# Performance work log

Measured on AMD Instinct MI355X. Metric: run time of the kernel, lower is better.

## Reference

```python
import jax, jax.numpy as jnp
import numpy as np

B, N, FEAT, D = 8, 2048, 64, 6
RADIUS, NSAMPLE, TOPK, NHEAD, NLAYER = 0.3, 64, 16, 8, 2
EPS = 1e-5


def _bn(x, p, axis=1):
    # eval-mode batchnorm; p rows = (gamma, beta, running_mean, running_var)
    g, b, m, v = p
    sh = [1] * x.ndim
    sh[axis] = -1
    rs = lambda t: t.reshape(sh)
    return (x - rs(m)) * (rs(g) / jnp.sqrt(rs(v) + EPS)) + rs(b)


def _ln(x, g, b):
    mu = jnp.mean(x, -1, keepdims=True)
    var = jnp.mean((x - mu) ** 2, -1, keepdims=True)
    return (x - mu) / jnp.sqrt(var + EPS) * g + b


def _mha(x, w_in, b_in, w_out, b_out):
    bsz, n, e = x.shape
    hd = e // NHEAD
    qkv = x @ w_in.T + b_in                      # [B,N,3E]
    q, k, v = jnp.split(qkv, 3, axis=-1)
    sp = lambda t: t.reshape(bsz, n, NHEAD, hd).transpose(0, 2, 1, 3)  # [B,H,N,hd]
    q, k, v = sp(q), sp(k), sp(v)
    att = jax.nn.softmax(jnp.einsum('bhnd,bhmd->bhnm', q, k) * (1.0 / hd ** 0.5), axis=-1)
    o = jnp.einsum('bhnm,bhmd->bhnd', att, v).transpose(0, 2, 1, 3).reshape(bsz, n, e)
    return o @ w_out.T + b_out


def _forward(sortvec, input, tl_win, tl_bin, tl_wout, tl_bout, tl_w1, tl_b1, tl_w2, tl_b2,
             tl_ln1g, tl_ln1b, tl_ln2g, tl_ln2b,
             fg_w0, fg_b0, fg_w1, fg_b1, fg_w2, fg_b2, fbn0, fbn1, fbn2,
             rc_w0, rc_b0, rc_w1, rc_b1, rc_w2, rc_b2, rbn0, rbn1, rbn2,
             fl_w0, fl_b0, fl_w1, fl_b1, lbn0, lbn1):
    b = sortvec.shape[0]
    n = sortvec.shape[-1]
    relu = jax.nn.relu

    # --- input self-attention (2 post-norm TransformerEncoder layers) ---
    x = sortvec[:, 0].transpose(0, 2, 1)         # [B,N,FEAT]
    for l in range(NLAYER):
        a = _mha(x, tl_win[l], tl_bin[l], tl_wout[l], tl_bout[l])
        x = _ln(x + a, tl_ln1g[l], tl_ln1b[l])
        f = relu(x @ tl_w1[l].T + tl_b1[l]) @ tl_w2[l].T + tl_b2[l]
        x = _ln(x + f, tl_ln2g[l], tl_ln2b[l])

    # --- feat_generator (RFFNet: Conv2d(FEAT,1) then 1x1 convs) + BN + relu ---
    s = jnp.einsum('cf,bnf->bcn', fg_w0, x) + fg_b0[:, None]   # [B,64,N]
    s = relu(_bn(s, fbn0))
    s = relu(_bn(jnp.einsum('co,bon->bcn', fg_w1, s) + fg_b1[:, None], fbn1))
    s = relu(_bn(jnp.einsum('co,bon->bcn', fg_w2, s) + fg_b2[:, None], fbn2))
    scores = s[:, 0]                              # [B,N]

    # --- top-k point selection ---
    _, idx = jax.lax.top_k(scores, TOPK)          # [B,K]
    all_points = input.transpose(0, 2, 1)         # [B,N,6]
    bidx = jnp.arange(b)[:, None]
    query = all_points[bidx, idx]                 # [B,K,6]

    # --- query_ball_point (PointNet++ style) ---
    xyz, qxyz = all_points[..., :3], query[..., :3]
    sqr = jnp.sum((qxyz[:, :, None, :] - xyz[:, None, :, :]) ** 2, -1)   # [B,K,N]
    gidx = jnp.where(sqr > RADIUS ** 2, n, jnp.arange(n)[None, None, :])
    gidx = jnp.sort(gidx, axis=-1)[..., :NSAMPLE]                        # [B,K,S]
    gidx = jnp.where(gidx == n, gidx[..., :1], gidx)
    radius_points = all_points[jnp.arange(b)[:, None, None], gidx]       # [B,K,S,6]
    grouped = jnp.concatenate([query[:, :, None, :], radius_points], axis=2)  # [B,K,S+1,6]

    # --- radius_cnn (Conv3d (1,S+1,6) then 1x1x1) + BN3d + relu ---
    r = jnp.einsum('cpd,bkpd->bck', rc_w0, grouped) + rc_b0[:, None]     # [B,128,K]
    r = relu(_bn(r, rbn0))
    r = relu(_bn(jnp.einsum('co,bok->bck', rc_w1, r) + rc_b1[:, None], rbn1))
    r = relu(_bn(jnp.einsum('co,bok->bck', rc_w2, r) + rc_b2[:, None], rbn2))  # [B,512,K]

    # --- flatten + Linear/BN1d/relu chain ---
    h = r.reshape(b, -1)                          # [B, 512*K]
    h = relu(_bn(h @ fl_w0.T + fl_b0, lbn0))
    h = relu(_bn(h @ fl_w1.T + fl_b1, lbn1))
    return h[..., None], idx                      # [B,512,1], [B,K]


def setup_inputs() -> dict:
    key = jax.random.key(0)
    ks = iter(jax.random.split(key, 80))
    rnd = lambda shape, s=0.02: jax.random.normal(next(ks), shape, jnp.float32) * s

    def bn_p(c):
        g = 1.0 + rnd((c,))
        bb = rnd((c,))
        m = rnd((c,))
        v = 1.0 + 0.1 * jnp.abs(rnd((c,), 1.0))
        return jnp.stack([g, bb, m, v])

    F = FEAT
    return dict(
        sortvec=jax.random.normal(next(ks), (B, 1, F, N), jnp.float32),
        input=jax.random.normal(next(ks), (B, D, N), jnp.float32),
        tl_win=rnd((NLAYER, 3 * F, F)), tl_bin=rnd((NLAYER, 3 * F)),
        tl_wout=rnd((NLAYER, F, F)), tl_bout=rnd((NLAYER, F)),
        tl_w1=rnd((NLAYER, 2048, F)), tl_b1=rnd((NLAYER, 2048)),
        tl_w2=rnd((NLAYER, F, 2048)), tl_b2=rnd((NLAYER, F)),
        tl_ln1g=jnp.ones((NLAYER, F)), tl_ln1b=jnp.zeros((NLAYER, F)),
        tl_ln2g=jnp.ones((NLAYER, F)), tl_ln2b=jnp.zeros((NLAYER, F)),
        fg_w0=rnd((64, F), 0.1), fg_b0=jnp.zeros((64,)),
        fg_w1=rnd((16, 64), 0.1), fg_b1=jnp.zeros((16,)),
        fg_w2=rnd((1, 16), 0.1), fg_b2=jnp.zeros((1,)),
        fbn0=bn_p(64), fbn1=bn_p(16), fbn2=bn_p(1),
        rc_w0=rnd((128, NSAMPLE + 1, D), 0.05), rc_b0=jnp.zeros((128,)),
        rc_w1=rnd((256, 128), 0.05), rc_b1=jnp.zeros((256,)),
        rc_w2=rnd((512, 256), 0.05), rc_b2=jnp.zeros((512,)),
        rbn0=bn_p(128), rbn1=bn_p(256), rbn2=bn_p(512),
        fl_w0=rnd((1024, 512 * TOPK), 0.02), fl_b0=jnp.zeros((1024,)),
        fl_w1=rnd((512, 1024), 0.02), fl_b1=jnp.zeros((512,)),
        lbn0=bn_p(1024), lbn1=bn_p(512),
    )


def reference(sortvec, input, tl_win, tl_bin, tl_wout, tl_bout, tl_w1, tl_b1, tl_w2, tl_b2,
              tl_ln1g, tl_ln1b, tl_ln2g, tl_ln2b,
              fg_w0, fg_b0, fg_w1, fg_b1, fg_w2, fg_b2, fbn0, fbn1, fbn2,
              rc_w0, rc_b0, rc_w1, rc_b1, rc_w2, rc_b2, rbn0, rbn1, rbn2,
              fl_w0, fl_b0, fl_w1, fl_b1, lbn0, lbn1):
    return _forward(sortvec, input, tl_win, tl_bin, tl_wout, tl_bout, tl_w1, tl_b1, tl_w2, tl_b2,
                    tl_ln1g, tl_ln1b, tl_ln2g, tl_ln2b,
                    fg_w0, fg_b0, fg_w1, fg_b1, fg_w2, fg_b2, fbn0, fbn1, fbn2,
                    rc_w0, rc_b0, rc_w1, rc_b1, rc_w2, rc_b2, rbn0, rbn1, rbn2,
                    fl_w0, fl_b0, fl_w1, fl_b1, lbn0, lbn1)
```

## Files before the change

### kernel.cpp

```cpp
#include <hip/hip_runtime.h>
#include <hip/hip_bf16.h>
#include <math.h>

#define BB 8
#define NN 2048
#define FF 64
#define DD 6
#define NSAMP 64
#define TOPK 16
#define NHEAD 8
#define HD 8
#define NLAYER 2
#define EPSF 1e-5f
#define R2 0.09f

typedef short short8 __attribute__((ext_vector_type(8)));
typedef float f32x4 __attribute__((ext_vector_type(4)));
typedef unsigned int u32;

__device__ inline unsigned pk2(float x) {
  unsigned b = __float_as_uint(x);
  unsigned hi = (b + 0x7fffu + ((b >> 16) & 1u)) >> 16;
  float r = x - __uint_as_float(hi << 16);
  unsigned c = __float_as_uint(r);
  unsigned lo = (c + 0x7fffu + ((c >> 16) & 1u)) >> 16;
  return (hi << 16) | lo;
}

__device__ inline unsigned short bf16r(float x) {
  unsigned b = __float_as_uint(x);
  return (unsigned short)((b + 0x7fffu + ((b >> 16) & 1u)) >> 16);
}

__device__ __forceinline__ void gl16(const void* g, void* l) {
  __builtin_amdgcn_global_load_lds((const __attribute__((address_space(1))) u32*)g,
                                   (__attribute__((address_space(3))) u32*)l, 16, 0, 0);
}

__global__ void k_transpose(const float* __restrict__ sv, float* __restrict__ x) {
  int i = blockIdx.x * 256 + threadIdx.x;
  if (i >= BB * NN * FF) return;
  int f = i % FF;
  int n = (i / FF) % NN;
  int b = i / (FF * NN);
  x[i] = sv[(b * FF + f) * NN + n];
}

__global__ void k_wimg(const float* __restrict__ w1, const float* __restrict__ w2,
                       unsigned short* __restrict__ img) {
  int i = blockIdx.x * 256 + threadIdx.x;
  int e = i & 4095;
  int plane = (i >> 12) & 3;
  int chg = (i >> 14) & 31;
  int l = i >> 19;
  int r = e >> 6, sh = (e >> 3) & 7, inner = e & 7;
  int s = sh ^ (r & 7);
  float v;
  if (plane < 2) v = w1[((size_t)(l * 2048 + chg * 64 + r)) * 64 + s * 8 + inner];
  else           v = w2[((size_t)(l * 64 + r)) * 2048 + chg * 64 + s * 8 + inner];
  unsigned p = pk2(v);
  img[i] = (unsigned short)((plane & 1) ? (p & 0xffffu) : (p >> 16));
}

__global__ void k_qkv3(const float* __restrict__ x, const float* __restrict__ win,
                       const float* __restrict__ bin, float* __restrict__ qbuf,
                       uint4* __restrict__ kp4, uint4* __restrict__ vp4) {
  __shared__ float xs[64 * 68];
  __shared__ float ws[64 * 68];
  int row0 = blockIdx.x * 64, y = blockIdx.y, col0 = y * 64;
  int t = threadIdx.x;
  #pragma unroll
  for (int i = 0; i < 4; ++i) {
    int q = t + i * 256, r = q >> 4, c = (q & 15) * 4;
    *(float4*)(xs + r * 68 + c) = *(const float4*)(x + (size_t)(row0 + r) * 64 + c);
    *(float4*)(ws + r * 68 + c) = *(const float4*)(win + (size_t)(col0 + r) * 64 + c);
  }
  __syncthreads();
  int tx = t & 15, ty = t >> 4;
  float acc[4][4] = {};
  for (int f = 0; f < 64; f += 4) {
    float4 xv[4], wv[4];
    #pragma unroll
    for (int ri = 0; ri < 4; ++ri) xv[ri] = *(const float4*)(xs + (ty * 4 + ri) * 68 + f);
    #pragma unroll
    for (int ci = 0; ci < 4; ++ci) wv[ci] = *(const float4*)(ws + (tx + 16 * ci) * 68 + f);
    #pragma unroll
    for (int ri = 0; ri < 4; ++ri)
      #pragma unroll
      for (int ci = 0; ci < 4; ++ci)
        acc[ri][ci] += xv[ri].x * wv[ci].x + xv[ri].y * wv[ci].y +
                       xv[ri].z * wv[ci].z + xv[ri].w * wv[ci].w;
  }
  int b = row0 >> 11, n0 = row0 & (NN - 1);
  if (y == 0) {
    #pragma unroll
    for (int ri = 0; ri < 4; ++ri)
      #pragma unroll
      for (int ci = 0; ci < 4; ++ci) {
        int r = row0 + ty * 4 + ri, c = tx + 16 * ci;
        qbuf[(size_t)r * 64 + c] = acc[ri][ci] + bin[c];
      }
    return;
  }
  __syncthreads();
  unsigned short* l16 = (unsigned short*)xs;
  if (y == 1) {
    #pragma unroll
    for (int ri = 0; ri < 4; ++ri)
      #pragma unroll
      for (int ci = 0; ci < 4; ++ci) {
        int r = ty * 4 + ri, c = tx + 16 * ci;
        l16[r * 72 + c] = bf16r(acc[ri][ci] + bin[64 + c]);
      }
    __syncthreads();
    #pragma unroll
    for (int i = 0; i < 2; ++i) {
      int idx = t + i * 256;
      int h = idx >> 6, tok = idx & 63;
      uint4 v = *(const uint4*)(l16 + tok * 72 + h * 8);
      kp4[(size_t)(b * NHEAD + h) * NN + n0 + tok] = v;
    }
  } else {
    #pragma unroll
    for (int ri = 0; ri < 4; ++ri)
      #pragma unroll
      for (int ci = 0; ci < 4; ++ci) {
        int r = ty * 4 + ri, c = tx + 16 * ci;
        l16[c * 72 + r] = bf16r(acc[ri][ci] + bin[128 + c]);
      }
    __syncthreads();
    #pragma unroll
    for (int i = 0; i < 2; ++i) {
      int idx = t + i * 256;
      int c = idx >> 3, seg = idx & 7;
      uint4 v = *(const uint4*)(l16 + c * 72 + seg * 8);
      vp4[(size_t)(b * 64 + c) * (NN / 8) + (n0 >> 3) + seg] = v;
    }
  }
}

__global__ void __launch_bounds__(256, 8)
k_attn7(const float* __restrict__ q, const uint4* __restrict__ kp4,
        const unsigned* __restrict__ vp32, float* __restrict__ a) {
  __shared__ uint4 kb4[256];
  __shared__ __attribute__((aligned(16))) unsigned short vb16[9 * 264];
  __shared__ __attribute__((aligned(16))) unsigned short pb16[4 * 16 * 40];
  int t = threadIdx.x;
  int lane = t & 63, w = t >> 6;
  int nIdx = lane & 15, lq = lane >> 4;
  int h = blockIdx.y, b = blockIdx.z;
  int qwb = blockIdx.x * 64 + w * 16;
  int bh = b * NHEAD + h;
  const float kf = 0.35355339059327373f * 1.4426950408889634f;
  short8 qF = {0, 0, 0, 0, 0, 0, 0, 0};
  if (lq == 0) {
    const float* qr = q + ((size_t)(b * NN + qwb + nIdx)) * 64 + h * HD;
    #pragma unroll
    for (int j = 0; j < 8; ++j) qF[j] = (short)bf16r(qr[j] * kf);
  }
  f32x4 acc = {0.f, 0.f, 0.f, 0.f};
  unsigned short* mypb = pb16 + w * 640;
  const uint4* kbase = kp4 + (size_t)bh * NN;
  const unsigned* vbase = vp32 + (size_t)bh * HD * (NN / 2);
  uint4 kreg = kbase[t];
  unsigned vreg[4];
  #pragma unroll
  for (int i = 0; i < 4; ++i) {
    int g = t + i * 256;
    vreg[i] = vbase[(g >> 7) * (NN / 2) + (g & 127)];
  }
  for (int kc = 0; kc < NN; kc += 256) {
    __syncthreads();
    kb4[t] = kreg;
    #pragma unroll
    for (int i = 0; i < 4; ++i) {
      int g = t + i * 256;
      ((unsigned*)vb16)[(g >> 7) * 132 + (g & 127)] = vreg[i];
    }
    if (t < 132) ((unsigned*)(vb16 + 8 * 264))[t] = 0x3f803f80u;
    __syncthreads();
    if (kc + 256 < NN) {
      kreg = kbase[kc + 256 + t];
      #pragma unroll
      for (int i = 0; i < 4; ++i) {
        int g = t + i * 256;
        vreg[i] = vbase[(g >> 7) * (NN / 2) + ((kc + 256) >> 1) + (g & 127)];
      }
    }
    for (int s = 0; s < 8; ++s) {
      int kb = s * 32;
      #pragma unroll
      for (int half = 0; half < 2; ++half) {
        int key = kb + half * 16 + nIdx;
        short8 bF = {0, 0, 0, 0, 0, 0, 0, 0};
        if (lq == 0) bF = *(const short8*)(kb4 + key);
        f32x4 c = {0.f, 0.f, 0.f, 0.f};
        c = __builtin_amdgcn_mfma_f32_16x16x32_bf16(qF, bF, c, 0, 0, 0);
        #pragma unroll
        for (int r = 0; r < 4; ++r) {
          float p = __builtin_amdgcn_exp2f(c[r]);
          mypb[(lq * 4 + r) * 40 + half * 16 + nIdx] =
              (unsigned short)(__float_as_uint(p) >> 16);
        }
      }
      short8 pa = *(const short8*)(mypb + nIdx * 40 + lq * 8);
      int vn = nIdx < 9 ? nIdx : 8;
      short8 vb = *(const short8*)(vb16 + vn * 264 + kb + lq * 8);
      acc = __builtin_amdgcn_mfma_f32_16x16x32_bf16(pa, vb, acc, 0, 0, 0);
    }
  }
  #pragma unroll
  for (int r = 0; r < 4; ++r) {
    float lr = __shfl(acc[r], (lane & 48) | 8);
    if (nIdx < 8) {
      int row = qwb + lq * 4 + r;
      a[((size_t)(b * NN + row)) * 64 + h * HD + nIdx] = acc[r] / lr;
    }
  }
}

__global__ void k_proj2(const float* __restrict__ a, const float* __restrict__ wout,
                        const float* __restrict__ bout, const float* __restrict__ g,
                        const float* __restrict__ be, float* __restrict__ x) {
  __shared__ float xs[64 * 68];
  __shared__ float ws[64 * 68];
  int row0 = blockIdx.x * 64;
  int t = threadIdx.x;
  #pragma unroll
  for (int i = 0; i < 4; ++i) {
    int q = t + i * 256, r = q >> 4, c = (q & 15) * 4;
    *(float4*)(xs + r * 68 + c) = *(const float4*)(a + (size_t)(row0 + r) * 64 + c);
    *(float4*)(ws + r * 68 + c) = *(const float4*)(wout + r * 64 + c);
  }
  __syncthreads();
  int tx = t & 15, ty = t >> 4;
  float acc[4][4] = {};
  for (int f = 0; f < 64; f += 4) {
    float4 xv[4], wv[4];
    #pragma unroll
    for (int ri = 0; ri < 4; ++ri) xv[ri] = *(const float4*)(xs + (ty * 4 + ri) * 68 + f);
    #pragma unroll
    for (int ci = 0; ci < 4; ++ci) wv[ci] = *(const float4*)(ws + (tx + 16 * ci) * 68 + f);
    #pragma unroll
    for (int ri = 0; ri < 4; ++ri)
      #pragma unroll
      for (int ci = 0; ci < 4; ++ci)
        acc[ri][ci] += xv[ri].x * wv[ci].x + xv[ri].y * wv[ci].y +
                       xv[ri].z * wv[ci].z + xv[ri].w * wv[ci].w;
  }
  #pragma unroll
  for (int ri = 0; ri < 4; ++ri) {
    int rl = ty * 4 + ri;
    float val[4], s = 0.f, sq = 0.f;
    #pragma unroll
    for (int ci = 0; ci < 4; ++ci) {
      int c = tx + 16 * ci;
      val[ci] = x[(size_t)(row0 + rl) * 64 + c] + bout[c] + acc[ri][ci];
      s += val[ci]; sq += val[ci] * val[ci];
    }
    #pragma unroll
    for (int off = 1; off < 16; off <<= 1) { s += __shfl_xor(s, off); sq += __shfl_xor(sq, off); }
    float mean = s * (1.f / 64.f);
    float var = sq * (1.f / 64.f) - mean * mean;
    float rstd = rsqrtf(var + EPSF);
    #pragma unroll
    for (int ci = 0; ci < 4; ++ci) {
      int c = tx + 16 * ci;
      x[(size_t)(row0 + rl) * 64 + c] = (val[ci] - mean) * rstd * g[c] + be[c];
    }
  }
}

__global__ void __launch_bounds__(256, 2)
k_ffn7(const float* __restrict__ x, const char* __restrict__ img,
       const float* __restrict__ b1, float* __restrict__ part) {
  __shared__ __attribute__((aligned(16))) char W1b[2][16384];
  __shared__ __attribute__((aligned(16))) char W2b[16384];
  __shared__ __attribute__((aligned(16))) unsigned short hpl[2][128 * 64];
  int row0 = blockIdx.x * 128;
  int ks = blockIdx.y, kc = ks * 512;
  int t = threadIdx.x, lane = t & 63, wv = t >> 6;
  int lm = lane & 15, lq = lane >> 4;
  const char* ibase = img + (size_t)ks * 8 * 32768;

  short8 axh[2][2], axl[2][2];
  #pragma unroll
  for (int m = 0; m < 2; ++m)
    #pragma unroll
    for (int kbi = 0; kbi < 2; ++kbi) {
      const float* xr = x + (size_t)(row0 + m * 64 + wv * 16 + lm) * 64 + kbi * 32 + lq * 8;
      #pragma unroll
      for (int j = 0; j < 8; ++j) {
        unsigned p = pk2(xr[j]);
        axh[m][kbi][j] = (short)(p >> 16);
        axl[m][kbi][j] = (short)(p & 0xffffu);
      }
    }
  float bv[8][4];
  #pragma unroll
  for (int ch = 0; ch < 8; ++ch)
    #pragma unroll
    for (int tn = 0; tn < 4; ++tn)
      bv[ch][tn] = b1[kc + ch * 64 + tn * 16 + lm];
  asm volatile("s_waitcnt vmcnt(0)" ::: "memory");
  __builtin_amdgcn_sched_barrier(0);
  #pragma unroll
  for (int i = 0; i < 4; ++i)
    gl16(ibase + i * 4096 + t * 16, &W1b[0][i * 4096 + t * 16]);

  f32x4 acc[2][4];
  #pragma unroll
  for (int m = 0; m < 2; ++m)
    #pragma unroll
    for (int tn = 0; tn < 4; ++tn) acc[m][tn] = (f32x4){0.f, 0.f, 0.f, 0.f};

  #pragma unroll
  for (int ch = 0; ch < 8; ++ch) {
    const int p = ch & 1;
    const char* cbase = ibase + ch * 32768;
    #pragma unroll
    for (int i = 0; i < 4; ++i)
      gl16(cbase + 16384 + i * 4096 + t * 16, &W2b[i * 4096 + t * 16]);
    if (ch < 7) {
      #pragma unroll
      for (int i = 0; i < 4; ++i)
        gl16(cbase + 32768 + i * 4096 + t * 16, &W1b[p ^ 1][i * 4096 + t * 16]);
    }
    if (ch < 7) { asm volatile("s_waitcnt vmcnt(8)" ::: "memory"); }
    else        { asm volatile("s_waitcnt vmcnt(4)" ::: "memory"); }
    __builtin_amdgcn_sched_barrier(0);
    __builtin_amdgcn_s_barrier();
    __builtin_amdgcn_sched_barrier(0);
    const char* P0h = W1b[p];
    const char* P0l = W1b[p] + 8192;
    f32x4 h4[2][4];
    #pragma unroll
    for (int m = 0; m < 2; ++m)
      #pragma unroll
      for (int tn = 0; tn < 4; ++tn) h4[m][tn] = (f32x4){0.f, 0.f, 0.f, 0.f};
    #pragma unroll
    for (int kbi = 0; kbi < 2; ++kbi) {
      int sw = (((kbi * 4 + lq) ^ (lm & 7)) << 4);
      #pragma unroll
      for (int tn = 0; tn < 4; ++tn) {
        int brow = tn * 16 + lm;
        short8 bhi = *(const short8*)(P0h + brow * 128 + sw);
        short8 blo = *(const short8*)(P0l + brow * 128 + sw);
        #pragma unroll
        for (int m = 0; m < 2; ++m) {
          h4[m][tn] = __builtin_amdgcn_mfma_f32_16x16x32_bf16(axh[m][kbi], bhi, h4[m][tn], 0, 0, 0);
          h4[m][tn] = __builtin_amdgcn_mfma_f32_16x16x32_bf16(axh[m][kbi], blo, h4[m][tn], 0, 0, 0);
          h4[m][tn] = __builtin_amdgcn_mfma_f32_16x16x32_bf16(axl[m][kbi], bhi, h4[m][tn], 0, 0, 0);
        }
      }
    }
    #pragma unroll
    for (int m = 0; m < 2; ++m)
      #pragma unroll
      for (int tn = 0; tn < 4; ++tn)
        #pragma unroll
        for (int r = 0; r < 4; ++r) {
          float hv = fmaxf(h4[m][tn][r] + bv[ch][tn], 0.f);
          unsigned u = __float_as_uint(hv);
          float resid = hv - __uint_as_float(u & 0xffff0000u);
          unsigned c2 = __float_as_uint(resid);
          int hrow = m * 64 + wv * 16 + lq * 4 + r, hcol = tn * 16 + lm;
          int off = hrow * 128 + (((hcol >> 3) ^ (hrow & 7)) << 4) + ((hcol & 7) << 1);
          *(unsigned short*)((char*)hpl[0] + off) = (unsigned short)(u >> 16);
          *(unsigned short*)((char*)hpl[1] + off) =
              (unsigned short)((c2 + 0x7fffu + ((c2 >> 16) & 1u)) >> 16);
        }
    if (ch < 7) { asm volatile("s_waitcnt vmcnt(4)" ::: "memory"); }
    else        { asm volatile("s_waitcnt vmcnt(0)" ::: "memory"); }
    __builtin_amdgcn_sched_barrier(0);
    __builtin_amdgcn_s_barrier();
    __builtin_amdgcn_sched_barrier(0);
    const char* P1h = W2b;
    const char* P1l = W2b + 8192;
    #pragma unroll
    for (int kbi = 0; kbi < 2; ++kbi) {
      short8 a2h[2], a2l[2];
      #pragma unroll
      for (int m = 0; m < 2; ++m) {
        int arow = m * 64 + wv * 16 + lm;
        int swa = (((kbi * 4 + lq) ^ (arow & 7)) << 4);
        a2h[m] = *(const short8*)((const char*)hpl[0] + arow * 128 + swa);
        a2l[m] = *(const short8*)((const char*)hpl[1] + arow * 128 + swa);
      }
      int swb = (((kbi * 4 + lq) ^ (lm & 7)) << 4);
      #pragma unroll
      for (int tn = 0; tn < 4; ++tn) {
        int brow = tn * 16 + lm;
        short8 bhi = *(const short8*)(P1h + brow * 128 + swb);
        short8 blo = *(const short8*)(P1l + brow * 128 + swb);
        #pragma unroll
        for (int m = 0; m < 2; ++m) {
          acc[m][tn] = __builtin_amdgcn_mfma_f32_16x16x32_bf16(a2h[m], bhi, acc[m][tn], 0, 0, 0);
          acc[m][tn] = __builtin_amdgcn_mfma_f32_16x16x32_bf16(a2h[m], blo, acc[m][tn], 0, 0, 0);
          acc[m][tn] = __builtin_amdgcn_mfma_f32_16x16x32_bf16(a2l[m], bhi, acc[m][tn], 0, 0, 0);
        }
      }
    }
    __builtin_amdgcn_s_barrier();
    __builtin_amdgcn_sched_barrier(0);
  }
  float* fb = (float*)hpl;
  #pragma unroll
  for (int m = 0; m < 2; ++m)
    #pragma unroll
    for (int tn = 0; tn < 4; ++tn)
      #pragma unroll
      for (int r = 0; r < 4; ++r) {
        int row = m * 64 + wv * 16 + lq * 4 + r;
        int col = (tn * 16 + lm) ^ ((row & 7) << 2);
        fb[row * 64 + col] = acc[m][tn][r];
      }
  __syncthreads();
  float* pb = part + (size_t)ks * (BB * NN * 64);
  #pragma unroll
  for (int i = 0; i < 8; ++i) {
    int idx = t * 4 + i * 1024;
    int row = idx >> 6, c0 = idx & 63;
    int c0s = c0 ^ ((row & 7) << 2);
    float4 v = *(const float4*)(fb + row * 64 + c0s);
    *(float4*)(pb + (size_t)(row0 + row) * 64 + c0) = v;
  }
}

__global__ void k_ffn_ln(const float* __restrict__ part, const float* __restrict__ b2,
                         const float* __restrict__ g, const float* __restrict__ be,
                         float* __restrict__ x) {
  int row = blockIdx.x * 4 + (threadIdx.x >> 6);
  int j = threadIdx.x & 63;
  size_t o = (size_t)row * 64 + j;
  const size_t S = (size_t)BB * NN * 64;
  float val = x[o] + b2[j] + ((part[o] + part[o + S]) + (part[o + 2 * S] + part[o + 3 * S]));
  float s = val;
  for (int off = 32; off; off >>= 1) s += __shfl_xor(s, off);
  s *= (1.f / 64.f);
  float d = val - s;
  float v = d * d;
  for (int off = 32; off; off >>= 1) v += __shfl_xor(v, off);
  v *= (1.f / 64.f);
  x[o] = d * rsqrtf(v + EPSF) * g[j] + be[j];
}

__global__ void k_fg2(const float* __restrict__ x,
                      const float* __restrict__ w0, const float* __restrict__ b0, const float* __restrict__ bn0,
                      const float* __restrict__ w1, const float* __restrict__ b1, const float* __restrict__ bn1,
                      const float* __restrict__ w2, const float* __restrict__ b2, const float* __restrict__ bn2,
                      float* __restrict__ scores) {
  __shared__ float xs[64 * 68];
  __shared__ float ws[64 * 68];
  __shared__ float s0s[64 * 68];
  __shared__ float s1s[64 * 20];
  int row0 = blockIdx.x * 64;
  int t = threadIdx.x;
  #pragma unroll
  for (int i = 0; i < 4; ++i) {
    int q = t + i * 256, r = q >> 4, c = (q & 15) * 4;
    *(float4*)(xs + r * 68 + c) = *(const float4*)(x + (size_t)(row0 + r) * 64 + c);
    *(float4*)(ws + r * 68 + c) = *(const float4*)(w0 + r * 64 + c);
  }
  __syncthreads();
  int tx = t & 15, ty = t >> 4;
  float acc[4][4] = {};
  for (int f = 0; f < 64; f += 4) {
    float4 xv[4], wv[4];
    #pragma unroll
    for (int ri = 0; ri < 4; ++ri) xv[ri] = *(const float4*)(xs + (ty * 4 + ri) * 68 + f);
    #pragma unroll
    for (int ci = 0; ci < 4; ++ci) wv[ci] = *(const float4*)(ws + (tx + 16 * ci) * 68 + f);
    #pragma unroll
    for (int ri = 0; ri < 4; ++ri)
      #pragma unroll
      for (int ci = 0; ci < 4; ++ci)
        acc[ri][ci] += xv[ri].x * wv[ci].x + xv[ri].y * wv[ci].y +
                       xv[ri].z * wv[ci].z + xv[ri].w * wv[ci].w;
  }
  #pragma unroll
  for (int ri = 0; ri < 4; ++ri)
    #pragma unroll
    for (int ci = 0; ci < 4; ++ci) {
      int c = tx + 16 * ci;
      float sc = bn0[c] * rsqrtf(bn0[192 + c] + EPSF);
      float v = (acc[ri][ci] + b0[c] - bn0[128 + c]) * sc + bn0[64 + c];
      s0s[(ty * 4 + ri) * 68 + c] = fmaxf(v, 0.f);
    }
  __syncthreads();
  {
    int rl = t & 63, j0 = t >> 6;
    #pragma unroll
    for (int i = 0; i < 4; ++i) {
      int j = j0 + 4 * i;
      float s = b1[j];
      const float* wr = w1 + j * 64;
      #pragma unroll 16
      for (int c = 0; c < 64; ++c) s += s0s[rl * 68 + c] * wr[c];
      float sc = bn1[j] * rsqrtf(bn1[48 + j] + EPSF);
      s = (s - bn1[32 + j]) * sc + bn1[16 + j];
      s1s[rl * 20 + j] = fmaxf(s, 0.f);
    }
  }
  __syncthreads();
  if (t < 64) {
    float s = b2[0];
    #pragma unroll
    for (int o = 0; o < 16; ++o) s += s1s[t * 20 + o] * w2[o];
    float sc = bn2[0] * rsqrtf(bn2[3] + EPSF);
    s = (s - bn2[2]) * sc + bn2[1];
    scores[row0 + t] = fmaxf(s, 0.f);
  }
}

__global__ void k_topk2(const float* __restrict__ scores, int* __restrict__ idx,
                        float* __restrict__ out_idx) {
  int b = blockIdx.x, t = threadIdx.x;
  float v[8];
  int base = b * NN;
  #pragma unroll
  for (int u = 0; u < 8; ++u) v[u] = scores[base + t + 256 * u];
  __shared__ float wvs[4];
  __shared__ int wis[4];
  __shared__ int winner;
  unsigned taken = 0;
  for (int r = 0; r < TOPK; ++r) {
    float best = -1e30f; int bi = 1 << 30;
    #pragma unroll
    for (int u = 0; u < 8; ++u) {
      if (!((taken >> u) & 1)) {
        float vv = v[u]; int ii = t + 256 * u;
        if (vv > best || (vv == best && ii < bi)) { best = vv; bi = ii; }
      }
    }
    for (int off = 32; off; off >>= 1) {
      float ov = __shfl_xor(best, off);
      int oi = __shfl_xor(bi, off);
      if (ov > best || (ov == best && oi < bi)) { best = ov; bi = oi; }
    }
    if ((t & 63) == 0) { wvs[t >> 6] = best; wis[t >> 6] = bi; }
    __syncthreads();
    if (t == 0) {
      float B = wvs[0]; int I = wis[0];
      #pragma unroll
      for (int q = 1; q < 4; ++q)
        if (wvs[q] > B || (wvs[q] == B && wis[q] < I)) { B = wvs[q]; I = wis[q]; }
      winner = I;
      idx[b * TOPK + r] = I;
      out_idx[b * TOPK + r] = (float)I;
    }
    __syncthreads();
    int w = winner;
    if ((w & 255) == t) taken |= 1u << (w >> 8);
  }
}

__global__ void __launch_bounds__(512)
k_group(const float* __restrict__ inp, const int* __restrict__ idx,
        const float* __restrict__ w0, const float* __restrict__ b0, const float* __restrict__ bn0,
        const float* __restrict__ w1, const float* __restrict__ b1, const float* __restrict__ bn1,
        const float* __restrict__ w2, const float* __restrict__ b2, const float* __restrict__ bn2,
        float* __restrict__ r2g) {
  __shared__ int swave[8 * 64];
  __shared__ int scnt[8];
  __shared__ int gidx[NSAMP];
  __shared__ __attribute__((aligned(16))) float gsh[65 * DD];
  __shared__ __attribute__((aligned(16))) float r0[128];
  __shared__ __attribute__((aligned(16))) float r1[256];
  int k = blockIdx.x, b = blockIdx.y;
  int t = threadIdx.x;
  int lane = t & 63, w = t >> 6;
  int qn = idx[b * TOPK + k];
  const float* px = inp + (size_t)b * DD * NN;
  float qx = px[qn], qy = px[NN + qn], qz = px[2 * NN + qn];
  {
    int cnt = 0;
    #pragma unroll
    for (int i = 0; i < 4; ++i) {
      int n = w * 256 + i * 64 + lane;
      float dx = px[n] - qx, dy = px[NN + n] - qy, dz = px[2 * NN + n] - qz;
      bool flag = (dx * dx + dy * dy + dz * dz <= R2);
      unsigned long long m = __ballot(flag);
      int pos = cnt + __popcll(m & ((1ull << lane) - 1ull));
      if (flag && pos < NSAMP) swave[w * 64 + pos] = n;
      cnt += (int)__popcll(m);
    }
    if (lane == 0) scnt[w] = cnt < NSAMP ? cnt : NSAMP;
  }
  __syncthreads();
  if (t < NSAMP) {
    int run = 0, val = -1;
    #pragma unroll
    for (int ww = 0; ww < 8; ++ww) {
      int c = scnt[ww];
      int loc = t - run;
      if (loc >= 0 && loc < c) val = swave[ww * 64 + loc];
      run += c;
    }
    gidx[t] = val;
  }
  __syncthreads();
  if (t < NSAMP) {
    int g0 = gidx[0];
    int gt = gidx[t];
    gidx[t] = (gt < 0) ? g0 : gt;
  }
  __syncthreads();
  if (t < 65 * DD) {
    int p = t / DD, d = t - p * DD;
    int n = (p == 0) ? qn : gidx[p - 1];
    gsh[t] = px[d * NN + n];
  }
  __syncthreads();
  {
    int c = t >> 2, part = t & 3;
    const float2* wr = (const float2*)(w0 + c * 390 + part * 98);
    const float2* gr = (const float2*)(gsh + part * 98);
    int n2 = (part == 3) ? 48 : 49;
    float s = 0.f;
    #pragma unroll 7
    for (int i = 0; i < n2; ++i) {
      float2 a = gr[i], ww = wr[i];
      s += a.x * ww.x + a.y * ww.y;
    }
    s += __shfl_xor(s, 1);
    s += __shfl_xor(s, 2);
    if (part == 0) {
      s += b0[c];
      float sc = bn0[c] * rsqrtf(bn0[384 + c] + EPSF);
      s = (s - bn0[256 + c]) * sc + bn0[128 + c];
      r0[c] = fmaxf(s, 0.f);
    }
  }
  __syncthreads();
  {
    int c = t >> 1, part = t & 1;
    const float4* wr = (const float4*)(w1 + c * 128 + part * 64);
    const float4* rr = (const float4*)(r0 + part * 64);
    float s0 = 0.f, s1 = 0.f, s2 = 0.f, s3 = 0.f;
    #pragma unroll 8
    for (int o = 0; o < 16; ++o) {
      float4 a = rr[o], ww = wr[o];
      s0 += a.x * ww.x; s1 += a.y * ww.y; s2 += a.z * ww.z; s3 += a.w * ww.w;
    }
    float s = (s0 + s1) + (s2 + s3);
    s += __shfl_xor(s, 1);
    if (part == 0) {
      s += b1[c];
      float sc = bn1[c] * rsqrtf(bn1[768 + c] + EPSF);
      s = (s - bn1[512 + c]) * sc + bn1[256 + c];
      r1[c] = fmaxf(s, 0.f);
    }
  }
  __syncthreads();
  {
    int c = t;
    const float4* wr = (const float4*)(w2 + c * 256);
    const float4* rr = (const float4*)r1;
    float s0 = 0.f, s1 = 0.f, s2 = 0.f, s3 = 0.f;
    #pragma unroll 8
    for (int o = 0; o < 64; ++o) {
      float4 a = rr[o], ww = wr[o];
      s0 += a.x * ww.x; s1 += a.y * ww.y; s2 += a.z * ww.z; s3 += a.w * ww.w;
    }
    float s = (s0 + s1) + (s2 + s3) + b2[c];
    float sc = bn2[c] * rsqrtf(bn2[1536 + c] + EPSF);
    s = (s - bn2[1024 + c]) * sc + bn2[512 + c];
    r2g[b * 8192 + c * TOPK + k] = fmaxf(s, 0.f);
  }
}

__global__ void k_fl(const float* __restrict__ hin, const float* __restrict__ w,
                     const float* __restrict__ bias, const float* __restrict__ bn,
                     float* __restrict__ hout, int IN, int OUT) {
  int blk = blockIdx.x;
  int b = blk / OUT, j = blk % OUT;
  int lane = threadIdx.x;
  const float* hr = hin + (size_t)b * IN;
  const float* wr = w + (size_t)j * IN;
  float s = 0.f;
  for (int i = lane; i < IN; i += 64) s += hr[i] * wr[i];
  for (int o = 32; o; o >>= 1) s += __shfl_xor(s, o);
  if (lane == 0) {
    s += bias[j];
    float sc = bn[j] * rsqrtf(bn[3 * OUT + j] + EPSF);
    s = (s - bn[2 * OUT + j]) * sc + bn[OUT + j];
    hout[b * OUT + j] = fmaxf(s, 0.f);
  }
}

extern "C" void kernel_launch(void* const* d_in, const int* in_sizes, int n_in,
                              void* d_out, int out_size, void* d_ws, size_t ws_size,
                              hipStream_t stream) {
  const float* sv      = (const float*)d_in[0];
  const float* inp     = (const float*)d_in[1];
  const float* tl_win  = (const float*)d_in[2];
  const float* tl_bin  = (const float*)d_in[3];
  const float* tl_wout = (const float*)d_in[4];
  const float* tl_bout = (const float*)d_in[5];
  const float* tl_w1   = (const float*)d_in[6];
  const float* tl_b1   = (const float*)d_in[7];
  const float* tl_w2   = (const float*)d_in[8];
  const float* tl_b2   = (const float*)d_in[9];
  const float* tl_ln1g = (const float*)d_in[10];
  const float* tl_ln1b = (const float*)d_in[11];
  const float* tl_ln2g = (const float*)d_in[12];
  const float* tl_ln2b = (const float*)d_in[13];
  const float* fg_w0   = (const float*)d_in[14];
  const float* fg_b0   = (const float*)d_in[15];
  const float* fg_w1   = (const float*)d_in[16];
  const float* fg_b1   = (const float*)d_in[17];
  const float* fg_w2   = (const float*)d_in[18];
  const float* fg_b2   = (const float*)d_in[19];
  const float* fbn0    = (const float*)d_in[20];
  const float* fbn1    = (const float*)d_in[21];
  const float* fbn2    = (const float*)d_in[22];
  const float* rc_w0   = (const float*)d_in[23];
  const float* rc_b0   = (const float*)d_in[24];
  const float* rc_w1   = (const float*)d_in[25];
  const float* rc_b1   = (const float*)d_in[26];
  const float* rc_w2   = (const float*)d_in[27];
  const float* rc_b2   = (const float*)d_in[28];
  const float* rbn0    = (const float*)d_in[29];
  const float* rbn1    = (const float*)d_in[30];
  const float* rbn2    = (const float*)d_in[31];
  const float* fl_w0   = (const float*)d_in[32];
  const float* fl_b0   = (const float*)d_in[33];
  const float* fl_w1   = (const float*)d_in[34];
  const float* fl_b1   = (const float*)d_in[35];
  const float* lbn0    = (const float*)d_in[36];
  const float* lbn1    = (const float*)d_in[37];
  (void)in_sizes; (void)n_in; (void)out_size; (void)ws_size;

  float* wsp = (float*)d_ws;
  float* x      = wsp;
  float* qkv    = x + BB * NN * FF;
  float* a      = qkv + BB * NN * 192;
  float* scores = a + BB * NN * FF;
  int*   idxb   = (int*)(scores + BB * NN);
  float* r2g    = (float*)(idxb + BB * TOPK);
  float* h1g    = r2g + BB * 8192;
  unsigned short* img = (unsigned short*)(h1g + BB * 1024);
  float* qbuf = qkv;
  unsigned short* kp = (unsigned short*)(qkv + BB * NN * FF);
  unsigned short* vp = kp + (size_t)BB * NHEAD * NN * HD;
  float* part = qkv;

  float* out = (float*)d_out;

  k_transpose<<<(BB * NN * FF) / 256, 256, 0, stream>>>(sv, x);
  k_wimg<<<(NLAYER * 32 * 4 * 4096) / 256, 256, 0, stream>>>(tl_w1, tl_w2, img);

  for (int l = 0; l < NLAYER; ++l) {
    k_qkv3<<<dim3(BB * NN / 64, 3), 256, 0, stream>>>(x, tl_win + l * 192 * FF,
                                                      tl_bin + l * 192, qbuf,
                                                      (uint4*)kp, (uint4*)vp);
    k_attn7<<<dim3(NN / 64, NHEAD, BB), 256, 0, stream>>>(qbuf, (const uint4*)kp,
                                                          (const unsigned*)vp, a);
    k_proj2<<<BB * NN / 64, 256, 0, stream>>>(a, tl_wout + l * FF * FF, tl_bout + l * FF,
                                              tl_ln1g + l * FF, tl_ln1b + l * FF, x);
    k_ffn7<<<dim3(BB * NN / 128, 4), 256, 0, stream>>>(x, (const char*)(img + (size_t)l * 524288),
                                                       tl_b1 + l * 2048, part);
    k_ffn_ln<<<BB * NN / 4, 256, 0, stream>>>(part, tl_b2 + l * FF,
                                              tl_ln2g + l * FF, tl_ln2b + l * FF, x);
  }

  k_fg2<<<BB * NN / 64, 256, 0, stream>>>(x, fg_w0, fg_b0, fbn0, fg_w1, fg_b1, fbn1,
                                          fg_w2, fg_b2, fbn2, scores);
  k_topk2<<<BB, 256, 0, stream>>>(scores, idxb, out + BB * 512);
  k_group<<<dim3(TOPK, BB), 512, 0, stream>>>(inp, idxb, rc_w0, rc_b0, rbn0,
                                              rc_w1, rc_b1, rbn1, rc_w2, rc_b2, rbn2, r2g);
  k_fl<<<BB * 1024, 64, 0, stream>>>(r2g, fl_w0, fl_b0, lbn0, h1g, 8192, 1024);
  k_fl<<<BB * 512, 64, 0, stream>>>(h1g, fl_w1, fl_b1, lbn1, out, 1024, 512);
}
```

Measured before the change: 506.4 us.

## Keep attention probabilities in registers via transposed MFMA and lane shuffles

```diff
diff --git a/kernel.cpp b/kernel.cpp
--- a/kernel.cpp
+++ b/kernel.cpp
@@ -16,6 +16,7 @@
 
 typedef short short8 __attribute__((ext_vector_type(8)));
 typedef float f32x4 __attribute__((ext_vector_type(4)));
+typedef unsigned uint4v __attribute__((ext_vector_type(4)));
 typedef unsigned int u32;
 
 __device__ inline unsigned pk2(float x) {
@@ -140,11 +141,10 @@
 }
 
 __global__ void __launch_bounds__(256, 8)
-k_attn7(const float* __restrict__ q, const uint4* __restrict__ kp4,
+k_attn8(const float* __restrict__ q, const uint4* __restrict__ kp4,
         const unsigned* __restrict__ vp32, float* __restrict__ a) {
   __shared__ uint4 kb4[256];
   __shared__ __attribute__((aligned(16))) unsigned short vb16[9 * 264];
-  __shared__ __attribute__((aligned(16))) unsigned short pb16[4 * 16 * 40];
   int t = threadIdx.x;
   int lane = t & 63, w = t >> 6;
   int nIdx = lane & 15, lq = lane >> 4;
@@ -159,9 +159,11 @@
     for (int j = 0; j < 8; ++j) qF[j] = (short)bf16r(qr[j] * kf);
   }
   f32x4 acc = {0.f, 0.f, 0.f, 0.f};
-  unsigned short* mypb = pb16 + w * 640;
   const uint4* kbase = kp4 + (size_t)bh * NN;
   const unsigned* vbase = vp32 + (size_t)bh * HD * (NN / 2);
+  int vn = nIdx < 9 ? nIdx : 8;
+  int voff = ((lq & 1) << 4) + ((lq >> 1) << 3);
+  if (t < 132) ((unsigned*)(vb16 + 8 * 264))[t] = 0x3f803f80u;
   uint4 kreg = kbase[t];
   unsigned vreg[4];
   #pragma unroll
@@ -177,7 +179,6 @@
       int g = t + i * 256;
       ((unsigned*)vb16)[(g >> 7) * 132 + (g & 127)] = vreg[i];
     }
-    if (t < 132) ((unsigned*)(vb16 + 8 * 264))[t] = 0x3f803f80u;
     __syncthreads();
     if (kc + 256 < NN) {
       kreg = kbase[kc + 256 + t];
@@ -189,33 +190,42 @@
     }
     for (int s = 0; s < 8; ++s) {
       int kb = s * 32;
+      unsigned pk_[4];
       #pragma unroll
       for (int half = 0; half < 2; ++half) {
         int key = kb + half * 16 + nIdx;
-        short8 bF = {0, 0, 0, 0, 0, 0, 0, 0};
-        if (lq == 0) bF = *(const short8*)(kb4 + key);
+        short8 aK = {0, 0, 0, 0, 0, 0, 0, 0};
+        if (lq == 0) aK = *(const short8*)(kb4 + key);
         f32x4 c = {0.f, 0.f, 0.f, 0.f};
-        c = __builtin_amdgcn_mfma_f32_16x16x32_bf16(qF, bF, c, 0, 0, 0);
-        #pragma unroll
-        for (int r = 0; r < 4; ++r) {
-          float p = __builtin_amdgcn_exp2f(c[r]);
-          mypb[(lq * 4 + r) * 40 + half * 16 + nIdx] =
-              (unsigned short)(__float_as_uint(p) >> 16);
-        }
-      }
-      short8 pa = *(const short8*)(mypb + nIdx * 40 + lq * 8);
-      int vn = nIdx < 9 ? nIdx : 8;
-      short8 vb = *(const short8*)(vb16 + vn * 264 + kb + lq * 8);
-      acc = __builtin_amdgcn_mfma_f32_16x16x32_bf16(pa, vb, acc, 0, 0, 0);
-    }
-  }
-  #pragma unroll
-  for (int r = 0; r < 4; ++r) {
-    float lr = __shfl(acc[r], (lane & 48) | 8);
-    if (nIdx < 8) {
-      int row = qwb + lq * 4 + r;
-      a[((size_t)(b * NN + row)) * 64 + h * HD + nIdx] = acc[r] / lr;
-    }
+        c = __builtin_amdgcn_mfma_f32_16x16x32_bf16(aK, qF, c, 0, 0, 0);
+        unsigned u0 = __float_as_uint(__builtin_amdgcn_exp2f(c[0]));
+        unsigned u1 = __float_as_uint(__builtin_amdgcn_exp2f(c[1]));
+        unsigned u2 = __float_as_uint(__builtin_amdgcn_exp2f(c[2]));
+        unsigned u3 = __float_as_uint(__builtin_amdgcn_exp2f(c[3]));
+        pk_[half * 2]     = (u0 >> 16) | (u1 & 0xffff0000u);
+        pk_[half * 2 + 1] = (u2 >> 16) | (u3 & 0xffff0000u);
+      }
+      unsigned e0 = (unsigned)__shfl_xor((int)pk_[0], 16);
+      unsigned e1 = (unsigned)__shfl_xor((int)pk_[1], 16);
+      unsigned e2 = (unsigned)__shfl_xor((int)pk_[2], 16);
+      unsigned e3 = (unsigned)__shfl_xor((int)pk_[3], 16);
+      bool odd = (lq & 1);
+      uint4v bw;
+      bw[0] = odd ? e2 : pk_[0];
+      bw[1] = odd ? e3 : pk_[1];
+      bw[2] = odd ? pk_[2] : e0;
+      bw[3] = odd ? pk_[3] : e1;
+      short8 bP = *(short8*)&bw;
+      short8 aV = *(const short8*)(vb16 + vn * 264 + kb + voff);
+      acc = __builtin_amdgcn_mfma_f32_16x16x32_bf16(aV, bP, acc, 0, 0, 0);
+    }
+  }
+  float lr = __shfl(acc[0], 32 + nIdx);
+  if (lq < 2) {
+    int row = qwb + nIdx;
+    float4 o;
+    o.x = acc[0] / lr; o.y = acc[1] / lr; o.z = acc[2] / lr; o.w = acc[3] / lr;
+    *(float4*)(a + ((size_t)(b * NN + row)) * 64 + h * HD + lq * 4) = o;
   }
 }
 
@@ -755,7 +765,7 @@
     k_qkv3<<<dim3(BB * NN / 64, 3), 256, 0, stream>>>(x, tl_win + l * 192 * FF,
                                                       tl_bin + l * 192, qbuf,
                                                       (uint4*)kp, (uint4*)vp);
-    k_attn7<<<dim3(NN / 64, NHEAD, BB), 256, 0, stream>>>(qbuf, (const uint4*)kp,
+    k_attn8<<<dim3(NN / 64, NHEAD, BB), 256, 0, stream>>>(qbuf, (const uint4*)kp,
                                                           (const unsigned*)vp, a);
     k_proj2<<<BB * NN / 64, 256, 0, stream>>>(a, tl_wout + l * FF * FF, tl_bout + l * FF,
                                               tl_ln1g + l * FF, tl_ln1b + l * FF, x);
```

After: 469.3 us. 7.3% less time.
